# Kernel tuning notes

Hardware: AMD Instinct MI355X
Metric: run time of the kernel (lower is better)

The kernel has to match this reference:

```python
import jax, jax.numpy as jnp
import numpy as np

B, T, E, H = 8, 2048, 1024, 64

def setup_inputs() -> dict:
    key = jax.random.key(0)
    kx, kk, kq, kv = jax.random.split(key, 4)
    x = jax.random.normal(kx, (B, T, E), dtype=jnp.float32)
    # nn.Linear(n_embd, head_size, bias=False): weight (H, E); store as (E, H) for x @ W
    Wk = jax.random.normal(kk, (E, H), dtype=jnp.float32) / np.sqrt(E)
    Wq = jax.random.normal(kq, (E, H), dtype=jnp.float32) / np.sqrt(E)
    Wv = jax.random.normal(kv, (E, H), dtype=jnp.float32) / np.sqrt(E)
    return {"x": x, "Wk": Wk, "Wq": Wq, "Wv": Wv}

def reference(x, Wk, Wq, Wv):
    # Single causal self-attention head (dropout in eval mode = identity).
    Bd, Td, Ed = x.shape
    k = x @ Wk  # [B,T,H]
    q = x @ Wq  # [B,T,H]
    v = x @ Wv  # [B,T,H]
    scale = jnp.asarray(64, x.dtype) ** -0.5  # hardcoded E2=64 in source
    wei = jnp.einsum('bth,bsh->bts', q, k) * scale  # [B,T,T]
    causal = jnp.tril(jnp.ones((Td, Td), dtype=bool))
    wei = jnp.where(causal, wei, -jnp.inf)
    wei = jax.nn.softmax(wei, axis=-1)
    out = jnp.einsum('bts,bsh->bth', wei, v)  # [B,T,H]
    return out
```

## Files before the change

kernel.cpp:

```cpp
#include <hip/hip_runtime.h>
#include <hip/hip_bf16.h>


typedef float f32x4 __attribute__((ext_vector_type(4)));
typedef float f32x16 __attribute__((ext_vector_type(16)));
typedef short bf16x8 __attribute__((ext_vector_type(8)));
typedef short bf16x4 __attribute__((ext_vector_type(4)));
typedef unsigned u32x2 __attribute__((ext_vector_type(2)));

#define MFMA16 __builtin_amdgcn_mfma_f32_16x16x32_bf16
#define MFMA32 __builtin_amdgcn_mfma_f32_32x32x16_bf16

__device__ __forceinline__ short f2bf(float f) {
    union { float f; unsigned u; } c; c.f = f;
    unsigned u = c.u;
    return (short)((u + 0x7FFFu + ((u >> 16) & 1u)) >> 16);
}

__device__ __forceinline__ unsigned cvt_pk_bf16(float lo, float hi) {
    unsigned r;
    asm("v_cvt_pk_bf16_f32 %0, %1, %2" : "=v"(r) : "v"(lo), "v"(hi));
    return r;
}

__global__ __launch_bounds__(256) void prep_w(const float* __restrict__ Wk,
                                              const float* __restrict__ Wq,
                                              const float* __restrict__ Wv,
                                              short* __restrict__ wsT) {
    int idx = blockIdx.x * 256 + threadIdx.x;
    int r = idx >> 10;
    int k = idx & 1023;
    int mat = r >> 6, c = r & 63;
    const float* W = (mat == 0) ? Wk : (mat == 1) ? Wq : Wv;
    float v = W[k * 64 + c];
    if (mat == 1) v *= 0.125f * 1.44269504088896f;
    wsT[r * 1024 + k] = f2bf(v);
}

__global__ __launch_bounds__(256) void proj(const float* __restrict__ x,
                                            const short* __restrict__ wsT,
                                            short* __restrict__ kF,
                                            short* __restrict__ qF,
                                            short* __restrict__ vF) {
    __shared__ char ldsraw[2 * 8192 + 2 * 24576];
    int tid = threadIdx.x;
    int w = tid >> 6, lane = tid & 63;
    int wm = w >> 1, wn = w & 1;
    int lr = lane & 15, lg = lane >> 4;
    int t0 = blockIdx.x * 32;

    f32x4 acc[6] = {};

    auto stage = [&](int kt, int buf) {
        int k0 = kt * 64;
#pragma unroll
        for (int s = 0; s < 2; ++s) {
            int G = s * 256 + tid;
            int row = G >> 4, p = G & 15;
            int g = p ^ (row & 15);
            const float* gp = x + (size_t)(t0 + row) * 1024 + k0 + g * 4;
            unsigned base = (unsigned)(buf * 8192 + s * 4096 + w * 1024);
            __builtin_amdgcn_global_load_lds(
                (const __attribute__((address_space(1))) void*)gp,
                (__attribute__((address_space(3))) void*)(ldsraw + base), 16, 0, 0);
        }
#pragma unroll
        for (int s = 0; s < 6; ++s) {
            int G = s * 256 + tid;
            int row = G >> 3, p = G & 7;
            int g = p ^ (row & 7);
            const short* gp = wsT + (size_t)row * 1024 + k0 + g * 8;
            unsigned base = (unsigned)(16384 + buf * 24576 + s * 4096 + w * 1024);
            __builtin_amdgcn_global_load_lds(
                (const __attribute__((address_space(1))) void*)gp,
                (__attribute__((address_space(3))) void*)(ldsraw + base), 16, 0, 0);
        }
    };

    int arow = wm * 16 + lr;

    stage(0, 0);
    __syncthreads();

    for (int kt = 0; kt < 16; ++kt) {
        int cur = kt & 1;
        if (kt < 15) stage(kt + 1, cur ^ 1);

        const char* xb = ldsraw + cur * 8192 + arow * 256;
        const char* wb = ldsraw + 16384 + cur * 24576;
#pragma unroll
        for (int ks = 0; ks < 2; ++ks) {
            int g0 = ks * 8 + lg * 2;
            f32x4 u0 = *(const f32x4*)(xb + ((g0)     ^ lr) * 16);
            f32x4 u1 = *(const f32x4*)(xb + ((g0 + 1) ^ lr) * 16);
            bf16x8 a;
#pragma unroll
            for (int j = 0; j < 4; ++j) { a[j] = f2bf(u0[j]); a[4 + j] = f2bf(u1[j]); }
            int slot = (ks * 4 + lg) ^ (lr & 7);
#pragma unroll
            for (int nt = 0; nt < 6; ++nt) {
                int brow = wn * 96 + nt * 16 + lr;
                bf16x8 bf = *(const bf16x8*)(wb + brow * 128 + slot * 16);
                acc[nt] = MFMA16(a, bf, acc[nt], 0, 0, 0);
            }
        }
        __syncthreads();
    }

    int tg = t0 + wm * 16 + lg * 4;
    int b = tg >> 11;
    int s = (tg & 2047) >> 5;
    int w32b = tg & 31;
#pragma unroll
    for (int nt = 0; nt < 6; ++nt) {
        int col0 = wn * 96 + nt * 16;
        int mat = col0 >> 6;
        int h = (col0 & 63) + lr;
        if (mat == 2) {
            int ht = h >> 5;
            int c = w32b >> 4;
            int hi2 = (lg >> 1) & 1;
            int jb = (lg & 1) * 4;
            int lanep = hi2 * 32 + (h & 31);
            bf16x4 pk;
#pragma unroll
            for (int r = 0; r < 4; ++r) pk[r] = f2bf(acc[nt][r]);
            size_t idx = (((((size_t)b * 64 + s) * 2 + ht) * 2 + c) * 64 + lanep) * 8 + jb;
            *(bf16x4*)(vF + idx) = pk;
        } else {
            short* dst = mat ? qF : kF;
            int c = h >> 4, hi2 = (h >> 3) & 1, j = h & 7;
            size_t base = ((((size_t)b * 64 + s) * 4 + c) * 64 + hi2 * 32) * 8 + j;
#pragma unroll
            for (int r = 0; r < 4; ++r)
                dst[base + (size_t)(w32b + r) * 8] = f2bf(acc[nt][r]);
        }
    }
}

__global__ __launch_bounds__(512, 4) void attn(const short* __restrict__ kF,
                                               const short* __restrict__ qF,
                                               const short* __restrict__ vF,
                                               float* __restrict__ out) {
    int bid = blockIdx.x;
    int b = bid & 7;
    int i = bid >> 3;
    int ti = (i & 1) ? (63 - (i >> 1)) : (i >> 1);
    int t0 = ti * 32;

    int w = threadIdx.x >> 6;
    int lane = threadIdx.x & 63;
    int q = lane & 31, hi = lane >> 5;

    __shared__ float lacc[8][32][65];
    __shared__ float lm[8][32], ll[8][32];

    const short* qp = qF + ((size_t)(b * 64 + ti)) * 2048 + lane * 8;
    bf16x8 qf0 = *(const bf16x8*)(qp);
    bf16x8 qf1 = *(const bf16x8*)(qp + 512);
    bf16x8 qf2 = *(const bf16x8*)(qp + 1024);
    bf16x8 qf3 = *(const bf16x8*)(qp + 1536);

    const short* kb_b = kF + (size_t)b * 64 * 2048 + lane * 8;
    const short* vb_b = vF + (size_t)b * 64 * 2048 + lane * 8;

    f32x16 acc0 = {}, acc1 = {};
    float m_s = -1e30f, l_s = 0.f;

    int nblk = ti + 1;
    for (int blk = w; blk < nblk; blk += 8) {
        const short* kp = kb_b + (size_t)blk * 2048;
        bf16x8 kf0 = *(const bf16x8*)(kp);
        bf16x8 kf1 = *(const bf16x8*)(kp + 512);
        bf16x8 kf2 = *(const bf16x8*)(kp + 1024);
        bf16x8 kf3 = *(const bf16x8*)(kp + 1536);

        f32x16 S = {};
        S = MFMA32(kf0, qf0, S, 0, 0, 0);
        S = MFMA32(kf1, qf1, S, 0, 0, 0);
        S = MFMA32(kf2, qf2, S, 0, 0, 0);
        S = MFMA32(kf3, qf3, S, 0, 0, 0);

        const short* vp = vb_b + (size_t)blk * 2048;
        bf16x8 vf00 = *(const bf16x8*)(vp);
        bf16x8 vf01 = *(const bf16x8*)(vp + 512);
        bf16x8 vf10 = *(const bf16x8*)(vp + 1024);
        bf16x8 vf11 = *(const bf16x8*)(vp + 1536);

        if (blk == ti) {
#pragma unroll
            for (int r = 0; r < 16; ++r) {
                int row = (r & 3) + 8 * (r >> 2) + 4 * hi;
                if (row > q) S[r] = -1e30f;
            }
        }

        float tm = S[0];
#pragma unroll
        for (int r = 1; r < 16; ++r) tm = fmaxf(tm, S[r]);
        tm = fmaxf(tm, __shfl_xor(tm, 32));
        float mn = fmaxf(m_s, tm);
        float fr = exp2f(m_s - mn);
        float p[16];
        float rs = 0.f;
#pragma unroll
        for (int r = 0; r < 16; ++r) { p[r] = exp2f(S[r] - mn); rs += p[r]; }
        rs += __shfl_xor(rs, 32);
        l_s = l_s * fr + rs;
        m_s = mn;

        unsigned pk0 = cvt_pk_bf16(p[0],  p[1]);
        unsigned pk1 = cvt_pk_bf16(p[2],  p[3]);
        unsigned pk2 = cvt_pk_bf16(p[4],  p[5]);
        unsigned pk3 = cvt_pk_bf16(p[6],  p[7]);
        unsigned pk4 = cvt_pk_bf16(p[8],  p[9]);
        unsigned pk5 = cvt_pk_bf16(p[10], p[11]);
        unsigned pk6 = cvt_pk_bf16(p[12], p[13]);
        unsigned pk7 = cvt_pk_bf16(p[14], p[15]);
        u32x2 s02 = __builtin_amdgcn_permlane32_swap(pk0, pk2, false, false);
        u32x2 s13 = __builtin_amdgcn_permlane32_swap(pk1, pk3, false, false);
        u32x2 s46 = __builtin_amdgcn_permlane32_swap(pk4, pk6, false, false);
        u32x2 s57 = __builtin_amdgcn_permlane32_swap(pk5, pk7, false, false);
        union { bf16x8 v; unsigned u[4]; } f0, f1;
        f0.u[0] = s02.x; f0.u[1] = s13.x; f0.u[2] = s02.y; f0.u[3] = s13.y;
        f1.u[0] = s46.x; f1.u[1] = s57.x; f1.u[2] = s46.y; f1.u[3] = s57.y;

#pragma unroll
        for (int r = 0; r < 16; ++r) { acc0[r] *= fr; acc1[r] *= fr; }

        acc0 = MFMA32(vf00, f0.v, acc0, 0, 0, 0);
        acc0 = MFMA32(vf01, f1.v, acc0, 0, 0, 0);
        acc1 = MFMA32(vf10, f0.v, acc1, 0, 0, 0);
        acc1 = MFMA32(vf11, f1.v, acc1, 0, 0, 0);
    }

    if (hi == 0) { lm[w][q] = m_s; ll[w][q] = l_s; }
#pragma unroll
    for (int r = 0; r < 16; ++r) {
        int row = (r & 3) + 8 * (r >> 2) + 4 * hi;
        lacc[w][q][row]      = acc0[r];
        lacc[w][q][32 + row] = acc1[r];
    }
    __syncthreads();

    int tid = threadIdx.x;
#pragma unroll
    for (int e = 0; e < 4; ++e) {
        int elem = e * 512 + tid;
        int row = elem >> 6, col = elem & 63;
        float ms = lm[0][row];
#pragma unroll
        for (int j = 1; j < 8; ++j) ms = fmaxf(ms, lm[j][row]);
        float lsum = 0.f, asum = 0.f;
#pragma unroll
        for (int j = 0; j < 8; ++j) {
            float sj = exp2f(lm[j][row] - ms);
            lsum += ll[j][row] * sj;
            asum += lacc[j][row][col] * sj;
        }
        out[(size_t)(b * 2048 + t0 + row) * 64 + col] = asum / lsum;
    }
}

extern "C" void kernel_launch(void* const* d_in, const int* in_sizes, int n_in,
                              void* d_out, int out_size, void* d_ws, size_t ws_size,
                              hipStream_t stream) {
    (void)in_sizes; (void)n_in; (void)out_size; (void)ws_size;
    const float* x  = (const float*)d_in[0];
    const float* Wk = (const float*)d_in[1];
    const float* Wq = (const float*)d_in[2];
    const float* Wv = (const float*)d_in[3];
    float* out = (float*)d_out;

    char* ws = (char*)d_ws;
    short* wsT = (short*)(ws);
    short* kF  = (short*)(ws + (1u << 20));
    short* qF  = (short*)(ws + (3u << 20));
    short* vF  = (short*)(ws + (5u << 20));

    prep_w<<<768, 256, 0, stream>>>(Wk, Wq, Wv, wsT);
    proj  <<<512, 256, 0, stream>>>(x, wsT, kF, qF, vF);
    attn  <<<512, 512, 0, stream>>>(kF, qF, vF, out);
}
```

Baseline: 44.29 us.

## Use 512-thread projection blocks and skip softmax rescale when max unchanged

```diff
diff --git a/kernel.cpp b/kernel.cpp
--- a/kernel.cpp
+++ b/kernel.cpp
@@ -37,40 +37,39 @@
     wsT[r * 1024 + k] = f2bf(v);
 }
 
-__global__ __launch_bounds__(256) void proj(const float* __restrict__ x,
-                                            const short* __restrict__ wsT,
-                                            short* __restrict__ kF,
-                                            short* __restrict__ qF,
-                                            short* __restrict__ vF) {
+__global__ __launch_bounds__(512, 4) void proj(const float* __restrict__ x,
+                                               const short* __restrict__ wsT,
+                                               short* __restrict__ kF,
+                                               short* __restrict__ qF,
+                                               short* __restrict__ vF) {
     __shared__ char ldsraw[2 * 8192 + 2 * 24576];
     int tid = threadIdx.x;
     int w = tid >> 6, lane = tid & 63;
-    int wm = w >> 1, wn = w & 1;
+    int wm = w >> 2, wn = w & 3;
     int lr = lane & 15, lg = lane >> 4;
     int t0 = blockIdx.x * 32;
 
-    f32x4 acc[6] = {};
+    f32x4 acc[3] = {};
 
     auto stage = [&](int kt, int buf) {
         int k0 = kt * 64;
-#pragma unroll
-        for (int s = 0; s < 2; ++s) {
-            int G = s * 256 + tid;
+        {
+            int G = tid;
             int row = G >> 4, p = G & 15;
             int g = p ^ (row & 15);
             const float* gp = x + (size_t)(t0 + row) * 1024 + k0 + g * 4;
-            unsigned base = (unsigned)(buf * 8192 + s * 4096 + w * 1024);
+            unsigned base = (unsigned)(buf * 8192 + w * 1024);
             __builtin_amdgcn_global_load_lds(
                 (const __attribute__((address_space(1))) void*)gp,
                 (__attribute__((address_space(3))) void*)(ldsraw + base), 16, 0, 0);
         }
 #pragma unroll
-        for (int s = 0; s < 6; ++s) {
-            int G = s * 256 + tid;
+        for (int s = 0; s < 3; ++s) {
+            int G = s * 512 + tid;
             int row = G >> 3, p = G & 7;
             int g = p ^ (row & 7);
             const short* gp = wsT + (size_t)row * 1024 + k0 + g * 8;
-            unsigned base = (unsigned)(16384 + buf * 24576 + s * 4096 + w * 1024);
+            unsigned base = (unsigned)(16384 + buf * 24576 + s * 8192 + w * 1024);
             __builtin_amdgcn_global_load_lds(
                 (const __attribute__((address_space(1))) void*)gp,
                 (__attribute__((address_space(3))) void*)(ldsraw + base), 16, 0, 0);
@@ -98,8 +97,8 @@
             for (int j = 0; j < 4; ++j) { a[j] = f2bf(u0[j]); a[4 + j] = f2bf(u1[j]); }
             int slot = (ks * 4 + lg) ^ (lr & 7);
 #pragma unroll
-            for (int nt = 0; nt < 6; ++nt) {
-                int brow = wn * 96 + nt * 16 + lr;
+            for (int nt = 0; nt < 3; ++nt) {
+                int brow = wn * 48 + nt * 16 + lr;
                 bf16x8 bf = *(const bf16x8*)(wb + brow * 128 + slot * 16);
                 acc[nt] = MFMA16(a, bf, acc[nt], 0, 0, 0);
             }
@@ -112,8 +111,8 @@
     int s = (tg & 2047) >> 5;
     int w32b = tg & 31;
 #pragma unroll
-    for (int nt = 0; nt < 6; ++nt) {
-        int col0 = wn * 96 + nt * 16;
+    for (int nt = 0; nt < 3; ++nt) {
+        int col0 = wn * 48 + nt * 16;
         int mat = col0 >> 6;
         int h = (col0 & 63) + lr;
         if (mat == 2) {
@@ -195,28 +194,46 @@
             }
         }
 
-        float tm = S[0];
-#pragma unroll
-        for (int r = 1; r < 16; ++r) tm = fmaxf(tm, S[r]);
+        float a0 = fmaxf(S[0], S[1]),   a1 = fmaxf(S[2], S[3]);
+        float a2 = fmaxf(S[4], S[5]),   a3 = fmaxf(S[6], S[7]);
+        float a4 = fmaxf(S[8], S[9]),   a5 = fmaxf(S[10], S[11]);
+        float a6 = fmaxf(S[12], S[13]), a7 = fmaxf(S[14], S[15]);
+        a0 = fmaxf(a0, a1); a2 = fmaxf(a2, a3);
+        a4 = fmaxf(a4, a5); a6 = fmaxf(a6, a7);
+        a0 = fmaxf(a0, a2); a4 = fmaxf(a4, a6);
+        float tm = fmaxf(a0, a4);
         tm = fmaxf(tm, __shfl_xor(tm, 32));
-        float mn = fmaxf(m_s, tm);
-        float fr = exp2f(m_s - mn);
-        float p[16];
-        float rs = 0.f;
-#pragma unroll
-        for (int r = 0; r < 16; ++r) { p[r] = exp2f(S[r] - mn); rs += p[r]; }
+
+        bool skip = __all(tm <= m_s);
+        float mn = skip ? m_s : fmaxf(m_s, tm);
+
+#pragma unroll
+        for (int r = 0; r < 16; ++r) S[r] = exp2f(S[r] - mn);
+        float b0 = (S[0] + S[1]) + (S[2] + S[3]);
+        float b1 = (S[4] + S[5]) + (S[6] + S[7]);
+        float b2 = (S[8] + S[9]) + (S[10] + S[11]);
+        float b3 = (S[12] + S[13]) + (S[14] + S[15]);
+        float rs = (b0 + b1) + (b2 + b3);
         rs += __shfl_xor(rs, 32);
-        l_s = l_s * fr + rs;
-        m_s = mn;
-
-        unsigned pk0 = cvt_pk_bf16(p[0],  p[1]);
-        unsigned pk1 = cvt_pk_bf16(p[2],  p[3]);
-        unsigned pk2 = cvt_pk_bf16(p[4],  p[5]);
-        unsigned pk3 = cvt_pk_bf16(p[6],  p[7]);
-        unsigned pk4 = cvt_pk_bf16(p[8],  p[9]);
-        unsigned pk5 = cvt_pk_bf16(p[10], p[11]);
-        unsigned pk6 = cvt_pk_bf16(p[12], p[13]);
-        unsigned pk7 = cvt_pk_bf16(p[14], p[15]);
+
+        if (skip) {
+            l_s += rs;
+        } else {
+            float fr = exp2f(m_s - mn);
+            l_s = l_s * fr + rs;
+            m_s = mn;
+#pragma unroll
+            for (int r = 0; r < 16; ++r) { acc0[r] *= fr; acc1[r] *= fr; }
+        }
+
+        unsigned pk0 = cvt_pk_bf16(S[0],  S[1]);
+        unsigned pk1 = cvt_pk_bf16(S[2],  S[3]);
+        unsigned pk2 = cvt_pk_bf16(S[4],  S[5]);
+        unsigned pk3 = cvt_pk_bf16(S[6],  S[7]);
+        unsigned pk4 = cvt_pk_bf16(S[8],  S[9]);
+        unsigned pk5 = cvt_pk_bf16(S[10], S[11]);
+        unsigned pk6 = cvt_pk_bf16(S[12], S[13]);
+        unsigned pk7 = cvt_pk_bf16(S[14], S[15]);
         u32x2 s02 = __builtin_amdgcn_permlane32_swap(pk0, pk2, false, false);
         u32x2 s13 = __builtin_amdgcn_permlane32_swap(pk1, pk3, false, false);
         u32x2 s46 = __builtin_amdgcn_permlane32_swap(pk4, pk6, false, false);
@@ -224,9 +241,6 @@
         union { bf16x8 v; unsigned u[4]; } f0, f1;
         f0.u[0] = s02.x; f0.u[1] = s13.x; f0.u[2] = s02.y; f0.u[3] = s13.y;
         f1.u[0] = s46.x; f1.u[1] = s57.x; f1.u[2] = s46.y; f1.u[3] = s57.y;
-
-#pragma unroll
-        for (int r = 0; r < 16; ++r) { acc0[r] *= fr; acc1[r] *= fr; }
 
         acc0 = MFMA32(vf00, f0.v, acc0, 0, 0, 0);
         acc0 = MFMA32(vf01, f1.v, acc0, 0, 0, 0);
@@ -279,6 +293,6 @@
     short* vF  = (short*)(ws + (5u << 20));
 
     prep_w<<<768, 256, 0, stream>>>(Wk, Wq, Wv, wsT);
-    proj  <<<512, 256, 0, stream>>>(x, wsT, kF, qF, vF);
+    proj  <<<512, 512, 0, stream>>>(x, wsT, kF, qF, vF);
     attn  <<<512, 512, 0, stream>>>(kF, qF, vF, out);
 }
```

Result: no change. 43.48 us (-1.8%).
